# Kernel tuning notes

Measured on AMD Instinct MI355X. Metric: run time of the kernel, lower is better.

The kernel has to match this reference:

```python
import jax, jax.numpy as jnp
import numpy as np

B, T, IN, H, L, OUT = 4096, 1024, 5, 16, 4, 150


def setup_inputs() -> dict:
    key = jax.random.key(0)
    ks = jax.random.split(key, 2 + 4 * L + 2)
    inp = {}
    inp["input_seq"] = jax.random.normal(ks[0], (B, T, IN), jnp.float32)
    inp["target_seq"] = jax.random.normal(ks[1], (B, 64, IN), jnp.float32)
    s = 1.0 / np.sqrt(H)  # PyTorch GRU init range
    i = 2
    for l in range(L):
        d = IN if l == 0 else H
        inp[f"W_ih{l}"] = jax.random.uniform(ks[i], (3 * H, d), jnp.float32, -s, s); i += 1
        inp[f"W_hh{l}"] = jax.random.uniform(ks[i], (3 * H, H), jnp.float32, -s, s); i += 1
        inp[f"b_ih{l}"] = jax.random.uniform(ks[i], (3 * H,), jnp.float32, -s, s); i += 1
        inp[f"b_hh{l}"] = jax.random.uniform(ks[i], (3 * H,), jnp.float32, -s, s); i += 1
    inp["fc_w"] = jax.random.uniform(ks[i], (OUT, L * H), jnp.float32, -s, s); i += 1
    inp["fc_b"] = jax.random.uniform(ks[i], (OUT,), jnp.float32, -s, s)
    return inp


def _gru_layer(x, W_ih, W_hh, b_ih, b_hh):
    # x: [B, T, d]. Precompute all input-side gate projections at once (one big GEMM).
    xg = jnp.einsum('btd,gd->btg', x, W_ih) + b_ih  # [B, T, 3H]
    h0 = jnp.zeros((x.shape[0], H), x.dtype)

    def step(h, xg_t):
        hg = h @ W_hh.T + b_hh                       # [B, 3H]
        xr, xz, xn = jnp.split(xg_t, 3, axis=-1)
        hr, hz, hn = jnp.split(hg, 3, axis=-1)
        r = jax.nn.sigmoid(xr + hr)
        z = jax.nn.sigmoid(xz + hz)
        n = jnp.tanh(xn + r * hn)
        h_new = (1.0 - z) * n + z * h
        return h_new, h_new

    hT, ys = jax.lax.scan(step, h0, jnp.swapaxes(xg, 0, 1))  # scan over time
    return jnp.swapaxes(ys, 0, 1), hT                        # [B,T,H], [B,H]


def reference(input_seq, target_seq,
              W_ih0, W_hh0, b_ih0, b_hh0,
              W_ih1, W_hh1, b_ih1, b_hh1,
              W_ih2, W_hh2, b_ih2, b_hh2,
              W_ih3, W_hh3, b_ih3, b_hh3,
              fc_w, fc_b):
    params = [(W_ih0, W_hh0, b_ih0, b_hh0), (W_ih1, W_hh1, b_ih1, b_hh1),
              (W_ih2, W_hh2, b_ih2, b_hh2), (W_ih3, W_hh3, b_ih3, b_hh3)]
    x = input_seq
    finals = []
    for (Wi, Wh, bi, bh) in params:
        x, hT = _gru_layer(x, Wi, Wh, bi, bh)
        finals.append(hT)
    # hidden: [L, B, H] -> rearrange 'l b h -> b (l h)'
    hidden = jnp.concatenate(finals, axis=-1)  # [B, L*H]
    return hidden @ fc_w.T + fc_b              # [B, 150]
```

## Files before the change

kernel.cpp:

```cpp
#include <hip/hip_runtime.h>

#define B_   4096
#define T_   1024
#define IN_  5
#define H_   16
#define L_   4
#define OUT_ 150
#define NB   16
#define LDW  12
#define SPI  8

typedef int      v4i  __attribute__((ext_vector_type(4)));
typedef int      v2i  __attribute__((ext_vector_type(2)));
typedef float    v4f  __attribute__((ext_vector_type(4)));
typedef float    f4   __attribute__((ext_vector_type(4)));
typedef _Float16 v8h  __attribute__((ext_vector_type(8)));

typedef v4i v4i_ma __attribute__((may_alias));
typedef v2i v2i_ma __attribute__((may_alias));
typedef f4  f4_ma  __attribute__((may_alias));

union Frag { v4i i; v8h h; };

__device__ __forceinline__ float fast_rcp(float x) { return __builtin_amdgcn_rcpf(x); }
__device__ __forceinline__ float sigm(float v) {
    float e = __expf(-v);
    return fast_rcp(1.0f + e);
}
__device__ __forceinline__ float tanh_fast(float v) {
    float e = __expf(-2.0f * fabsf(v));
    float t = (1.0f - e) * fast_rcp(1.0f + e);
    return copysignf(t, v);
}
__device__ __forceinline__ int pk(float a, float b) {
    return __builtin_bit_cast(int, __builtin_amdgcn_cvt_pkrtz(a, b));
}
__device__ __forceinline__ v4f mfma16h(v8h a, v8h b, v4f c) {
    return __builtin_amdgcn_mfma_f32_16x16x32_f16(a, b, c, 0, 0, 0);
}
__device__ __forceinline__ void barrier_lds() {
    asm volatile("s_waitcnt lgkmcnt(0)" ::: "memory");
    __builtin_amdgcn_s_barrier();
    asm volatile("" ::: "memory");
}

__global__ __launch_bounds__(256)
__attribute__((amdgpu_waves_per_eu(1, 1)))
void gru_tr(
    const float* __restrict__ x_in,
    const float* __restrict__ Wih0, const float* __restrict__ Whh0,
    const float* __restrict__ bih0, const float* __restrict__ bhh0,
    const float* __restrict__ Wih1, const float* __restrict__ Whh1,
    const float* __restrict__ bih1, const float* __restrict__ bhh1,
    const float* __restrict__ Wih2, const float* __restrict__ Whh2,
    const float* __restrict__ bih2, const float* __restrict__ bhh2,
    const float* __restrict__ Wih3, const float* __restrict__ Whh3,
    const float* __restrict__ bih3, const float* __restrict__ bhh3,
    const float* __restrict__ fcw,  const float* __restrict__ fcb,
    float* __restrict__ out)
{
    __shared__ int   hbuf[L_ - 1][2][SPI][NB * LDW];
    __shared__ float fchid[NB][L_ * H_];

    const int tid  = threadIdx.x;
    const int w    = tid >> 6;
    const int lane = tid & 63;
    const int q    = lane >> 4;
    const int mm   = lane & 15;
    const int b0   = blockIdx.x * NB;

    const float *wi, *wh, *bip, *bhp;
    if      (w == 0) { wi = Wih0; wh = Whh0; bip = bih0; bhp = bhh0; }
    else if (w == 1) { wi = Wih1; wh = Whh1; bip = bih1; bhp = bhh1; }
    else if (w == 2) { wi = Wih2; wh = Whh2; bip = bih2; bhp = bhh2; }
    else             { wi = Wih3; wh = Whh3; bip = bih3; bhp = bhh3; }
    const int KX = (w == 0) ? IN_ : H_;

    for (int i = tid; i < (L_ - 1) * 2 * SPI * NB * LDW; i += 256)
        (&hbuf[0][0][0][0])[i] = 0;

    Frag Af[4];
    v4f  cb[4];
    {
#pragma unroll
        for (int tile = 0; tile < 4; ++tile) {
            const int rowbase = (tile == 0) ? 0 : (tile == 1) ? 16 : 32;
            const int r = rowbase + mm;
            float vals[8];
#pragma unroll
            for (int e = 0; e < 8; ++e) {
                const int k = q * 8 + e;
                float v = 0.0f;
                if (k < 16) { if (tile != 3 && k < KX) v = wi[r * KX + k]; }
                else        { if (tile != 2)           v = wh[r * H_ + (k - 16)]; }
                vals[e] = v;
            }
#pragma unroll
            for (int d = 0; d < 4; ++d)
                Af[tile].i[d] = pk(vals[2 * d], vals[2 * d + 1]);
#pragma unroll
            for (int reg = 0; reg < 4; ++reg) {
                const int n = q * 4 + reg;
                float b;
                if      (tile == 0) b = bip[n] + bhp[n];
                else if (tile == 1) b = bip[16 + n] + bhp[16 + n];
                else if (tile == 2) b = bip[32 + n];
                else                b = bhp[32 + n];
                cb[tile][reg] = b;
            }
        }
    }
    __syncthreads();

    const float* xptr = x_in + (size_t)(b0 + mm) * T_ * IN_;
    float XA[5 * SPI], XB[5 * SPI];
#pragma unroll
    for (int c = 0; c < 5 * SPI; ++c) { XA[c] = 0.0f; XB[c] = 0.0f; }
    if (w == 0 && q == 0) {
#pragma unroll
        for (int c = 0; c < 10; ++c)
            ((f4*)XA)[c] = *(const f4_ma*)(xptr + 4 * c);
    }

    float hold[4] = {0.0f, 0.0f, 0.0f, 0.0f};
    int pkA = 0, pkB = 0;

    const int qq  = (q >= 2) ? (q - 2) : 0;
    const int s0l = (qq * 2) * 16 + mm;
    const int s1l = (qq * 2 + 1) * 16 + mm;

    const int NI = T_ / SPI + L_ - 1;

    auto body = [&](int k, float (&Xc)[5 * SPI], float (&Xn)[5 * SPI]) {
        const int t0 = SPI * (k - w);
        if (0 <= t0 && t0 < T_) {
            const int rp = (k - 1) & 1, wp = k & 1;

            Frag up[SPI];
            if (w > 0) {
#pragma unroll
                for (int s = 0; s < SPI; ++s)
                    up[s].i = *(const v4i_ma*)&hbuf[w - 1][rp][s][mm * LDW + (q & 1) * 4];
            }
            if (w == 0 && q == 0) {
                int tn0 = t0 + SPI; if (tn0 > T_ - SPI) tn0 = T_ - SPI;
                const float* xp = xptr + tn0 * IN_;
#pragma unroll
                for (int c = 0; c < 10; ++c)
                    ((f4*)Xn)[c] = *(const f4_ma*)(xp + 4 * c);
            }

#pragma unroll
            for (int s = 0; s < SPI; ++s) {
                int sh0 = __shfl(pkA, s0l, 64);
                int sh1 = __shfl(pkB, s0l, 64);
                int sh2 = __shfl(pkA, s1l, 64);
                int sh3 = __shfl(pkB, s1l, 64);

                Frag Bf;
                if (w == 0) {
                    int x0 = pk(Xc[5 * s + 0], Xc[5 * s + 1]);
                    int x1 = pk(Xc[5 * s + 2], Xc[5 * s + 3]);
                    int x2 = pk(Xc[5 * s + 4], 0.0f);
                    Bf.i[0] = (q >= 2) ? sh0 : ((q == 0) ? x0 : 0);
                    Bf.i[1] = (q >= 2) ? sh1 : ((q == 0) ? x1 : 0);
                    Bf.i[2] = (q >= 2) ? sh2 : ((q == 0) ? x2 : 0);
                    Bf.i[3] = (q >= 2) ? sh3 : 0;
                } else {
                    Bf.i[0] = (q >= 2) ? sh0 : up[s].i[0];
                    Bf.i[1] = (q >= 2) ? sh1 : up[s].i[1];
                    Bf.i[2] = (q >= 2) ? sh2 : up[s].i[2];
                    Bf.i[3] = (q >= 2) ? sh3 : up[s].i[3];
                }

                v4f a0 = mfma16h(Af[0].h, Bf.h, cb[0]);
                v4f a1 = mfma16h(Af[1].h, Bf.h, cb[1]);
                v4f a2 = mfma16h(Af[2].h, Bf.h, cb[2]);
                v4f a3 = mfma16h(Af[3].h, Bf.h, cb[3]);

#pragma unroll
                for (int reg = 0; reg < 4; ++reg) {
                    float r = sigm(a0[reg]);
                    float z = sigm(a1[reg]);
                    float n = tanh_fast(fmaf(r, a3[reg], a2[reg]));
                    float h = fmaf(z, hold[reg] - n, n);
                    hold[reg] = h;
                }
                pkA = pk(hold[0], hold[1]);
                pkB = pk(hold[2], hold[3]);

                if (w < 3)
                    *(v2i_ma*)&hbuf[w][wp][s][mm * LDW + q * 2] = (v2i){pkA, pkB};
            }
        }
        barrier_lds();
    };

#pragma unroll 1
    for (int k = 0; k + 1 < NI; k += 2) {
        body(k, XA, XB);
        body(k + 1, XB, XA);
    }
    body(NI - 1, XA, XB);

#pragma unroll
    for (int reg = 0; reg < 4; ++reg)
        fchid[mm][w * H_ + q * 4 + reg] = hold[reg];
    barrier_lds();

    for (int o = tid; o < NB * OUT_; o += 256) {
        const int m = o / OUT_, oc = o % OUT_;
        float acc = fcb[oc];
#pragma unroll
        for (int kk = 0; kk < L_ * H_; ++kk)
            acc = fmaf(fcw[oc * (L_ * H_) + kk], fchid[m][kk], acc);
        out[(size_t)(b0 + m) * OUT_ + oc] = acc;
    }
}

extern "C" void kernel_launch(void* const* d_in, const int* in_sizes, int n_in,
                              void* d_out, int out_size, void* d_ws, size_t ws_size,
                              hipStream_t stream) {
    const float* xin = (const float*)d_in[0];
    gru_tr<<<B_ / NB, 256, 0, stream>>>(
        xin,
        (const float*)d_in[2],  (const float*)d_in[3],  (const float*)d_in[4],  (const float*)d_in[5],
        (const float*)d_in[6],  (const float*)d_in[7],  (const float*)d_in[8],  (const float*)d_in[9],
        (const float*)d_in[10], (const float*)d_in[11], (const float*)d_in[12], (const float*)d_in[13],
        (const float*)d_in[14], (const float*)d_in[15], (const float*)d_in[16], (const float*)d_in[17],
        (const float*)d_in[18], (const float*)d_in[19],
        (float*)d_out);
}
```

Measured before the change: 406.0 us.

## Fold exp scaling into weights and replace shuffles with permlane swaps

The log2(e) and -2·log2(e) scale factors are pre-multiplied into the fp16 weight fragments and biases. The gate nonlinearities can then call exp2 directly, and tanh drops its abs/copysign. The four per-step ds_bpermute shuffles that rebuild the recurrent B fragment are replaced by v_permlane32_swap and v_permlane16_swap register swaps. This takes LDS-crossbar latency off the serial recurrence. In exchange, the fp16-rounded scaled weights change precision slightly, and the unclamped exp2 in tanh could overflow to inf for large negative inputs.

```diff
diff --git a/kernel.cpp b/kernel.cpp
--- a/kernel.cpp
+++ b/kernel.cpp
@@ -23,20 +23,24 @@
 union Frag { v4i i; v8h h; };
 
 __device__ __forceinline__ float fast_rcp(float x) { return __builtin_amdgcn_rcpf(x); }
-__device__ __forceinline__ float sigm(float v) {
-    float e = __expf(-v);
-    return fast_rcp(1.0f + e);
-}
-__device__ __forceinline__ float tanh_fast(float v) {
-    float e = __expf(-2.0f * fabsf(v));
-    float t = (1.0f - e) * fast_rcp(1.0f + e);
-    return copysignf(t, v);
+__device__ __forceinline__ float ex2(float x) {
+#if __has_builtin(__builtin_amdgcn_exp2f)
+    return __builtin_amdgcn_exp2f(x);
+#else
+    return exp2f(x);
+#endif
 }
 __device__ __forceinline__ int pk(float a, float b) {
     return __builtin_bit_cast(int, __builtin_amdgcn_cvt_pkrtz(a, b));
 }
 __device__ __forceinline__ v4f mfma16h(v8h a, v8h b, v4f c) {
     return __builtin_amdgcn_mfma_f32_16x16x32_f16(a, b, c, 0, 0, 0);
+}
+__device__ __forceinline__ void pswap16(int &a, int &b) {
+    asm("v_permlane16_swap_b32 %0, %1" : "+v"(a), "+v"(b));
+}
+__device__ __forceinline__ void pswap32(int &a, int &b) {
+    asm("v_permlane32_swap_b32 %0, %1" : "+v"(a), "+v"(b));
 }
 __device__ __forceinline__ void barrier_lds() {
     asm volatile("s_waitcnt lgkmcnt(0)" ::: "memory");
@@ -46,7 +50,7 @@
 
 __global__ __launch_bounds__(256)
 __attribute__((amdgpu_waves_per_eu(1, 1)))
-void gru_tr(
+void gru_pl2(
     const float* __restrict__ x_in,
     const float* __restrict__ Wih0, const float* __restrict__ Whh0,
     const float* __restrict__ bih0, const float* __restrict__ bhh0,
@@ -79,35 +83,36 @@
     for (int i = tid; i < (L_ - 1) * 2 * SPI * NB * LDW; i += 256)
         (&hbuf[0][0][0][0])[i] = 0;
 
+    const float SC_RZ = -1.4426950408889634f;
+    const float SC_N  = -2.8853900817779268f;
     Frag Af[4];
     v4f  cb[4];
-    {
-#pragma unroll
-        for (int tile = 0; tile < 4; ++tile) {
-            const int rowbase = (tile == 0) ? 0 : (tile == 1) ? 16 : 32;
-            const int r = rowbase + mm;
-            float vals[8];
-#pragma unroll
-            for (int e = 0; e < 8; ++e) {
-                const int k = q * 8 + e;
-                float v = 0.0f;
-                if (k < 16) { if (tile != 3 && k < KX) v = wi[r * KX + k]; }
-                else        { if (tile != 2)           v = wh[r * H_ + (k - 16)]; }
-                vals[e] = v;
-            }
-#pragma unroll
-            for (int d = 0; d < 4; ++d)
-                Af[tile].i[d] = pk(vals[2 * d], vals[2 * d + 1]);
-#pragma unroll
-            for (int reg = 0; reg < 4; ++reg) {
-                const int n = q * 4 + reg;
-                float b;
-                if      (tile == 0) b = bip[n] + bhp[n];
-                else if (tile == 1) b = bip[16 + n] + bhp[16 + n];
-                else if (tile == 2) b = bip[32 + n];
-                else                b = bhp[32 + n];
-                cb[tile][reg] = b;
-            }
+#pragma unroll
+    for (int tile = 0; tile < 4; ++tile) {
+        const float sc = (tile < 2) ? SC_RZ : SC_N;
+        const int rowbase = (tile == 0) ? 0 : (tile == 1) ? 16 : 32;
+        const int r = rowbase + mm;
+        float vals[8];
+#pragma unroll
+        for (int e = 0; e < 8; ++e) {
+            const int k = q * 8 + e;
+            float v = 0.0f;
+            if (k < 16) { if (tile != 3 && k < KX) v = wi[r * KX + k]; }
+            else        { if (tile != 2)           v = wh[r * H_ + (k - 16)]; }
+            vals[e] = v * sc;
+        }
+#pragma unroll
+        for (int d = 0; d < 4; ++d)
+            Af[tile].i[d] = pk(vals[2 * d], vals[2 * d + 1]);
+#pragma unroll
+        for (int reg = 0; reg < 4; ++reg) {
+            const int n = q * 4 + reg;
+            float b;
+            if      (tile == 0) b = bip[n] + bhp[n];
+            else if (tile == 1) b = bip[16 + n] + bhp[16 + n];
+            else if (tile == 2) b = bip[32 + n];
+            else                b = bhp[32 + n];
+            cb[tile][reg] = b * sc;
         }
     }
     __syncthreads();
@@ -124,10 +129,6 @@
 
     float hold[4] = {0.0f, 0.0f, 0.0f, 0.0f};
     int pkA = 0, pkB = 0;
-
-    const int qq  = (q >= 2) ? (q - 2) : 0;
-    const int s0l = (qq * 2) * 16 + mm;
-    const int s1l = (qq * 2 + 1) * 16 + mm;
 
     const int NI = T_ / SPI + L_ - 1;
 
@@ -152,25 +153,26 @@
 
 #pragma unroll
             for (int s = 0; s < SPI; ++s) {
-                int sh0 = __shfl(pkA, s0l, 64);
-                int sh1 = __shfl(pkB, s0l, 64);
-                int sh2 = __shfl(pkA, s1l, 64);
-                int sh3 = __shfl(pkB, s1l, 64);
+                int uA = pkA, vA = pkA; pswap32(uA, vA); pswap16(uA, vA);
+                int uB = pkB, vB = pkB; pswap32(uB, vB); pswap16(uB, vB);
 
                 Frag Bf;
-                if (w == 0) {
-                    int x0 = pk(Xc[5 * s + 0], Xc[5 * s + 1]);
-                    int x1 = pk(Xc[5 * s + 2], Xc[5 * s + 3]);
-                    int x2 = pk(Xc[5 * s + 4], 0.0f);
-                    Bf.i[0] = (q >= 2) ? sh0 : ((q == 0) ? x0 : 0);
-                    Bf.i[1] = (q >= 2) ? sh1 : ((q == 0) ? x1 : 0);
-                    Bf.i[2] = (q >= 2) ? sh2 : ((q == 0) ? x2 : 0);
-                    Bf.i[3] = (q >= 2) ? sh3 : 0;
-                } else {
-                    Bf.i[0] = (q >= 2) ? sh0 : up[s].i[0];
-                    Bf.i[1] = (q >= 2) ? sh1 : up[s].i[1];
-                    Bf.i[2] = (q >= 2) ? sh2 : up[s].i[2];
-                    Bf.i[3] = (q >= 2) ? sh3 : up[s].i[3];
+                {
+                    int l0, l1, l2, l3;
+                    if (w == 0) {
+                        l0 = (q == 0) ? pk(Xc[5 * s + 0], Xc[5 * s + 1]) : 0;
+                        l1 = (q == 0) ? pk(Xc[5 * s + 2], Xc[5 * s + 3]) : 0;
+                        l2 = (q == 0) ? pk(Xc[5 * s + 4], 0.0f)          : 0;
+                        l3 = 0;
+                    } else {
+                        l0 = up[s].i[0]; l1 = up[s].i[1];
+                        l2 = up[s].i[2]; l3 = up[s].i[3];
+                    }
+                    const bool hi = (q >= 2);
+                    Bf.i[0] = hi ? uA : l0;
+                    Bf.i[1] = hi ? uB : l1;
+                    Bf.i[2] = hi ? vA : l2;
+                    Bf.i[3] = hi ? vB : l3;
                 }
 
                 v4f a0 = mfma16h(Af[0].h, Bf.h, cb[0]);
@@ -180,11 +182,11 @@
 
 #pragma unroll
                 for (int reg = 0; reg < 4; ++reg) {
-                    float r = sigm(a0[reg]);
-                    float z = sigm(a1[reg]);
-                    float n = tanh_fast(fmaf(r, a3[reg], a2[reg]));
-                    float h = fmaf(z, hold[reg] - n, n);
-                    hold[reg] = h;
+                    float r = fast_rcp(1.0f + ex2(a0[reg]));
+                    float z = fast_rcp(1.0f + ex2(a1[reg]));
+                    float e = ex2(fmaf(r, a3[reg], a2[reg]));
+                    float n = (1.0f - e) * fast_rcp(1.0f + e);
+                    hold[reg] = fmaf(z, hold[reg] - n, n);
                 }
                 pkA = pk(hold[0], hold[1]);
                 pkB = pk(hold[2], hold[3]);
@@ -222,7 +224,7 @@
                               void* d_out, int out_size, void* d_ws, size_t ws_size,
                               hipStream_t stream) {
     const float* xin = (const float*)d_in[0];
-    gru_tr<<<B_ / NB, 256, 0, stream>>>(
+    gru_pl2<<<B_ / NB, 256, 0, stream>>>(
         xin,
         (const float*)d_in[2],  (const float*)d_in[3],  (const float*)d_in[4],  (const float*)d_in[5],
         (const float*)d_in[6],  (const float*)d_in[7],  (const float*)d_in[8],  (const float*)d_in[9],
```

After: 353.0 us. -13.0%, faster.
